# Optimization experiments

Measured on AMD Instinct MI355X. Metric: run time of the kernel, lower is better.

The kernel has to match this reference:

```python
import jax, jax.numpy as jnp
import numpy as np
import math

B, S, H, NH, HD, RD, INNER, MAXPOS, EPS = 2, 2048, 4096, 16, 256, 64, 16384, 2048, 1e-5


def setup_inputs() -> dict:
    key = jax.random.key(0)
    ks = jax.random.split(key, 8)
    sd = 0.02
    return {
        "hidden_states": jax.random.normal(ks[0], (B, S, H), jnp.float32),
        "attention_mask": jnp.ones((B, S), jnp.int32),
        "position_ids": jnp.broadcast_to(jnp.arange(S, dtype=jnp.int32), (B, S)),
        "ln_scale": jnp.ones((H,), jnp.float32),
        "ln_bias": jnp.zeros((H,), jnp.float32),
        "wq": jax.random.normal(ks[1], (H, H), jnp.float32) * sd,
        "wk": jax.random.normal(ks[2], (H, H), jnp.float32) * sd,
        "wv": jax.random.normal(ks[3], (H, H), jnp.float32) * sd,
        "wo": jax.random.normal(ks[4], (H, H), jnp.float32) * sd,
        "w_in": jax.random.normal(ks[5], (H, INNER), jnp.float32) * sd,
        "b_in": jnp.zeros((INNER,), jnp.float32),
        "w_out": jax.random.normal(ks[6], (INNER, H), jnp.float32) * sd,
        "b_out": jnp.zeros((H,), jnp.float32),
    }


def _rotate_every_two(t):
    # interleave (-odd, even) pairs along last dim
    r = jnp.stack((-t[..., 1::2], t[..., ::2]), axis=-1)
    return r.reshape(t.shape)


def reference(hidden_states, attention_mask, position_ids, ln_scale, ln_bias,
              wq, wk, wv, wo, w_in, b_in, w_out, b_out):
    x = hidden_states
    # LayerNorm (single ln feeds both attn and mlp in GPT-J parallel block)
    mu = jnp.mean(x, axis=-1, keepdims=True)
    var = jnp.mean(jnp.square(x - mu), axis=-1, keepdims=True)
    h = (x - mu) * jax.lax.rsqrt(var + EPS) * ln_scale + ln_bias

    # QKV projections (no bias), split heads: [B,S,NH,HD]
    q = (h @ wq).reshape(B, S, NH, HD)
    k = (h @ wk).reshape(B, S, NH, HD)
    v = (h @ wv).reshape(B, S, NH, HD)

    # sinusoidal table over rotary_dim, gathered by position_ids
    pos = jnp.arange(MAXPOS, dtype=jnp.float32)
    inv_freq = 1.0 / (10000.0 ** (jnp.arange(0, RD, 2, dtype=jnp.float32) / RD))
    freqs = pos[:, None] * inv_freq[None, :]          # [MAXPOS, RD//2]
    table = jnp.concatenate([jnp.sin(freqs), jnp.cos(freqs)], axis=-1)  # [MAXPOS, RD]
    sincos = table[position_ids]                      # [B,S,RD]
    sin, cos = jnp.split(sincos, 2, axis=-1)          # each [B,S,RD//2]
    sinr = jnp.repeat(sin[:, :, None, :], 2, axis=3)  # [B,S,1,RD]
    cosr = jnp.repeat(cos[:, :, None, :], 2, axis=3)

    def rope(t):
        return t * cosr + _rotate_every_two(t) * sinr

    q = jnp.concatenate([rope(q[..., :RD]), q[..., RD:]], axis=-1)
    k = jnp.concatenate([rope(k[..., :RD]), k[..., RD:]], axis=-1)

    # combined causal + padding mask -> additive bias
    causal = jnp.tril(jnp.ones((S, S), dtype=bool))
    mask = (attention_mask[:, None, None, :] > 0) & causal[None, None, :, :]
    bias = jnp.where(mask, 0.0, jnp.finfo(jnp.float32).min)  # [B,1,S,S]

    scale = 1.0 / math.sqrt(HD)
    scores = jnp.einsum('bqhd,bkhd->bhqk', q, k) * scale + bias
    attn = jax.nn.softmax(scores, axis=-1)
    ctx = jnp.einsum('bhqk,bkhd->bqhd', attn, v).reshape(B, S, H)
    attn_out = ctx @ wo

    # MLP on the same LN output (parallel residual), gelu_new ~ tanh gelu
    mlp = jax.nn.gelu(h @ w_in + b_in, approximate=True) @ w_out + b_out

    return x + attn_out + mlp
```

## Files before the change

### kernel.cpp

```cpp
#include <hip/hip_runtime.h>
#include <hip/hip_bf16.h>
#include <math.h>

namespace {

constexpr int kB = 2;
constexpr int kS = 2048;
constexpr int kH = 4096;
constexpr int kNH = 16;
constexpr int kHD = 256;
constexpr int kLDQ = 12288;

typedef __attribute__((ext_vector_type(4))) float f32x4;
typedef __attribute__((ext_vector_type(8))) short bf16x8;

__device__ __forceinline__ unsigned short f2bf(float f) {
  unsigned int u = __float_as_uint(f);
  u += 0x7FFFu + ((u >> 16) & 1u);
  return (unsigned short)(u >> 16);
}
__device__ __forceinline__ float bf2f(unsigned short h) {
  return __uint_as_float(((unsigned int)h) << 16);
}
__device__ __forceinline__ void gl2lds16(const void* g, void* l) {
  __builtin_amdgcn_global_load_lds(
      (const __attribute__((address_space(1))) unsigned int*)g,
      (__attribute__((address_space(3))) unsigned int*)l, 16, 0, 0);
}

#define SBAR asm volatile("s_barrier" ::: "memory")
#define LGKM0 asm volatile("s_waitcnt lgkmcnt(0)" ::: "memory")

__global__ __launch_bounds__(256) void ln_fwd(
    const float* __restrict__ x, const float* __restrict__ gam,
    const float* __restrict__ bet, unsigned short* __restrict__ hout,
    float* __restrict__ outp) {
  int row = blockIdx.x;
  int t = threadIdx.x;
  const float4* xr = (const float4*)(x + (size_t)row * kH);
  float4 v[4];
  float sum = 0.f, sq = 0.f;
#pragma unroll
  for (int i = 0; i < 4; i++) {
    v[i] = xr[t + i * 256];
    sum += v[i].x + v[i].y + v[i].z + v[i].w;
    sq += v[i].x * v[i].x + v[i].y * v[i].y + v[i].z * v[i].z + v[i].w * v[i].w;
  }
#pragma unroll
  for (int o = 32; o > 0; o >>= 1) {
    sum += __shfl_xor(sum, o);
    sq += __shfl_xor(sq, o);
  }
  __shared__ float red[8];
  if ((t & 63) == 0) { red[t >> 6] = sum; red[4 + (t >> 6)] = sq; }
  __syncthreads();
  sum = red[0] + red[1] + red[2] + red[3];
  sq = red[4] + red[5] + red[6] + red[7];
  float mu = sum * (1.f / kH);
  float rstd = rsqrtf(sq * (1.f / kH) - mu * mu + 1e-5f);
  const float4* gp = (const float4*)gam;
  const float4* bp = (const float4*)bet;
  ushort4* hr = (ushort4*)(hout + (size_t)row * kH);
  float4* orow = (float4*)(outp + (size_t)row * kH);
#pragma unroll
  for (int i = 0; i < 4; i++) {
    float4 g = gp[t + i * 256];
    float4 bb = bp[t + i * 256];
    ushort4 hv;
    hv.x = f2bf((v[i].x - mu) * rstd * g.x + bb.x);
    hv.y = f2bf((v[i].y - mu) * rstd * g.y + bb.y);
    hv.z = f2bf((v[i].z - mu) * rstd * g.z + bb.z);
    hv.w = f2bf((v[i].w - mu) * rstd * g.w + bb.w);
    hr[t + i * 256] = hv;
    orow[t + i * 256] = v[i];
  }
}

__global__ __launch_bounds__(256) void cvt_t(
    const float* __restrict__ in, int ldin, unsigned short* __restrict__ outp,
    int ldout) {
  __shared__ float tile[32][33];
  int n0 = blockIdx.x * 32, k0 = blockIdx.y * 32;
  int tx = threadIdx.x, ty = threadIdx.y;
#pragma unroll
  for (int i = 0; i < 4; i++)
    tile[ty + i * 8][tx] = in[(size_t)(k0 + ty + i * 8) * ldin + n0 + tx];
  __syncthreads();
#pragma unroll
  for (int i = 0; i < 4; i++)
    outp[(size_t)(n0 + ty + i * 8) * ldout + k0 + tx] =
        f2bf(tile[tx][ty + i * 8]);
}

__global__ __launch_bounds__(256) void vtrans(
    const unsigned short* __restrict__ qkv, unsigned short* __restrict__ vt) {
  __shared__ unsigned short tile[32][33];
  int bh = blockIdx.z;
  int s0 = blockIdx.x * 32, d0 = blockIdx.y * 32;
  int tx = threadIdx.x, ty = threadIdx.y;
  int b = bh >> 4, h = bh & 15;
  const unsigned short* src =
      qkv + (size_t)(b * kS) * kLDQ + 8192 + h * kHD;
#pragma unroll
  for (int i = 0; i < 4; i++)
    tile[ty + i * 8][tx] = src[(size_t)(s0 + ty + i * 8) * kLDQ + d0 + tx];
  __syncthreads();
  unsigned short* dst = vt + (size_t)bh * kHD * kS;
#pragma unroll
  for (int i = 0; i < 4; i++)
    dst[(size_t)(d0 + ty + i * 8) * kS + s0 + tx] = tile[tx][ty + i * 8];
}

__global__ __launch_bounds__(256) void rope_scale(
    unsigned short* __restrict__ qkv, const int* __restrict__ pos) {
  int idx = blockIdx.x * 256 + threadIdx.x;
  int j = idx & 127;
  int rowh = idx >> 7;
  int h = rowh & 15;
  int s = (rowh >> 4) & 2047;
  int b = rowh >> 15;
  size_t off = ((size_t)(b * kS + s)) * kLDQ + h * kHD + 2 * j;
  const float SCALE = 0.0625f;
  if (j < 32) {
    int p = pos[b * kS + s];
    float inv = exp2f(-(float)j * (13.287712379549449f / 32.f));
    float fr = (float)p * inv;
    float sn, cs;
    sincosf(fr, &sn, &cs);
    float e = bf2f(qkv[off]), o = bf2f(qkv[off + 1]);
    qkv[off] = f2bf((e * cs - o * sn) * SCALE);
    qkv[off + 1] = f2bf((o * cs + e * sn) * SCALE);
    e = bf2f(qkv[off + 4096]); o = bf2f(qkv[off + 4097]);
    qkv[off + 4096] = f2bf(e * cs - o * sn);
    qkv[off + 4097] = f2bf(o * cs + e * sn);
  } else {
    qkv[off] = f2bf(bf2f(qkv[off]) * SCALE);
    qkv[off + 1] = f2bf(bf2f(qkv[off + 1]) * SCALE);
  }
}

#define AF_MMA(P)                                                           \
  {                                                                         \
    bf16x8 af_[2][2];                                                       \
    _Pragma("unroll") for (int fm = 0; fm < 2; fm++)                        \
        _Pragma("unroll") for (int kk = 0; kk < 2; kk++) {                  \
      int q_ = (2 * (P) + fm) * 16 + l15;                                   \
      af_[fm][kk] = *(const bf16x8*)(cur + ((q_ & 64) << 8) + wm * 8192 +   \
                                     ((q_ & 63) << 7) +                     \
                                     ((((kk << 2) | l4) ^ key) << 4));      \
    }                                                                       \
    __builtin_amdgcn_s_setprio(1);                                          \
    _Pragma("unroll") for (int fm = 0; fm < 2; fm++)                        \
        _Pragma("unroll") for (int fn = 0; fn < 4; fn++)                    \
            _Pragma("unroll") for (int kk = 0; kk < 2; kk++)                \
      acc[2 * (P) + fm][fn] = __builtin_amdgcn_mfma_f32_16x16x32_bf16(      \
          af_[fm][kk], bfr[fn][kk], acc[2 * (P) + fm][fn], 0, 0, 0);        \
    __builtin_amdgcn_s_setprio(0);                                          \
  }

template <int EPI>
__global__ __launch_bounds__(512, 2) void gemm256(
    const unsigned short* __restrict__ A, int lda,
    const unsigned short* __restrict__ Bt, int ldb, void* __restrict__ Cp,
    int ldc, const float* __restrict__ bias, int K, int gx) {
  __shared__ __align__(16) char lds[131072];
  const int t = threadIdx.x;
  const int lane = t & 63, w = t >> 6;
  const int wm = w >> 2, wn = w & 3;
  const int l15 = lane & 15, l4 = lane >> 4;
  const int key = l15 & 7;

  const int nwg = gridDim.x;
  const int orig = blockIdx.x;
  const int wg = (orig & 7) * (nwg >> 3) + (orig >> 3);
  const int bx = wg % gx, by = wg / gx;
  const int m0 = by * 256, n0 = bx * 256;

  const int lr = t >> 3, ch = t & 7;
  const int swk = (ch ^ (lr & 7)) * 8;
  const unsigned short* aE0 = A + (size_t)(m0 + lr) * lda + swk;
  const unsigned short* aE1 = A + (size_t)(m0 + 128 + lr) * lda + swk;
  const unsigned short* aL0 = A + (size_t)(m0 + 64 + lr) * lda + swk;
  const unsigned short* aL1 = A + (size_t)(m0 + 192 + lr) * lda + swk;
  const unsigned short* b00 = Bt + (size_t)(n0 + lr) * ldb + swk;
  const unsigned short* b01 = Bt + (size_t)(n0 + 64 + lr) * ldb + swk;
  const unsigned short* b10 = Bt + (size_t)(n0 + 128 + lr) * ldb + swk;
  const unsigned short* b11 = Bt + (size_t)(n0 + 192 + lr) * ldb + swk;
  const int t16 = t * 16;

  f32x4 acc[8][4];
#pragma unroll
  for (int m = 0; m < 8; m++)
#pragma unroll
    for (int n = 0; n < 4; n++) acc[m][n] = (f32x4)(0.f);

  {
    char* b = lds;
    gl2lds16(b00, b + 32768 + t16); b00 += 64;
    gl2lds16(b01, b + 40960 + t16); b01 += 64;
    gl2lds16(b10, b + 49152 + t16); b10 += 64;
    gl2lds16(b11, b + 57344 + t16); b11 += 64;
    gl2lds16(aE0, b + t16);         aE0 += 64;
    gl2lds16(aE1, b + 8192 + t16);  aE1 += 64;
    gl2lds16(aL0, b + 16384 + t16); aL0 += 64;
    gl2lds16(aL1, b + 24576 + t16); aL1 += 64;
  }
  asm volatile("s_waitcnt vmcnt(2)" ::: "memory");
  SBAR;

  const int nt = K >> 6;
  for (int kt = 0; kt < nt; ++kt) {
    const char* cur = lds + (kt & 1) * 65536;
    char* nxt = lds + (((kt & 1) ^ 1)) * 65536;
    const bool pre = (kt + 1 < nt);
    bf16x8 bfr[4][2];
    if (pre) {
      gl2lds16(b00, nxt + 32768 + t16); b00 += 64;
      gl2lds16(b01, nxt + 40960 + t16); b01 += 64;
      gl2lds16(b10, nxt + 49152 + t16); b10 += 64;
      gl2lds16(b11, nxt + 57344 + t16); b11 += 64;
    }
#pragma unroll
    for (int fn = 0; fn < 4; fn++)
#pragma unroll
      for (int kk = 0; kk < 2; kk++) {
        int n = wn * 64 + fn * 16 + l15;
        bfr[fn][kk] = *(const bf16x8*)(cur + 32768 + (n << 7) +
                                       ((((kk << 2) | l4) ^ key) << 4));
      }
    AF_MMA(0)
    if (pre) {
      gl2lds16(aE0, nxt + t16);         aE0 += 64;
      gl2lds16(aE1, nxt + 8192 + t16);  aE1 += 64;
      gl2lds16(aL0, nxt + 16384 + t16); aL0 += 64;
      gl2lds16(aL1, nxt + 24576 + t16); aL1 += 64;
    }
    AF_MMA(1)
    if (pre) asm volatile("s_waitcnt vmcnt(8)" ::: "memory");
    else     asm volatile("s_waitcnt vmcnt(0)" ::: "memory");
    SBAR;
    AF_MMA(2)
    AF_MMA(3)
    LGKM0;
    if (pre) asm volatile("s_waitcnt vmcnt(2)" ::: "memory");
    SBAR;
  }

  const int crow = m0 + wm * 128 + l4 * 4;
  const int ccol = n0 + wn * 64 + l15;
#pragma unroll
  for (int m = 0; m < 8; m++) {
#pragma unroll
    for (int n = 0; n < 4; n++) {
      int col = ccol + n * 16;
#pragma unroll
      for (int r = 0; r < 4; r++) {
        int row = crow + m * 16 + r;
        float v = acc[m][n][r];
        size_t idx = (size_t)row * ldc + col;
        if constexpr (EPI == 0) {
          ((unsigned short*)Cp)[idx] = f2bf(v);
        } else if constexpr (EPI == 1) {
          float u = v + bias[col];
          float c = 0.7978845608028654f * (u + 0.044715f * u * u * u);
          float g = u / (1.0f + __expf(-2.0f * c));
          ((unsigned short*)Cp)[idx] = f2bf(g);
        } else if constexpr (EPI == 2) {
          ((float*)Cp)[idx] += v;
        } else {
          ((float*)Cp)[idx] += v + bias[col];
        }
      }
    }
  }
}

__global__ __launch_bounds__(512) void attn_fwd(
    const unsigned short* __restrict__ qkv, const unsigned short* __restrict__ vt,
    const int* __restrict__ amask, unsigned short* __restrict__ ctx) {
  __shared__ __align__(16) char alds[147456];
  const int t = threadIdx.x, lane = t & 63, w = t >> 6;
  const int bid = blockIdx.x;
  const int qb = 15 - (bid >> 5);
  const int bh = bid & 31;
  const int b = bh >> 4, h = bh & 15;
  const int l15 = lane & 15, l4 = lane >> 4;
  const int qbase = qb * 128;

  bf16x8 qf[8];
  {
    int qrow = qbase + w * 16 + l15;
    const unsigned short* qp =
        qkv + (size_t)(b * kS + qrow) * kLDQ + h * kHD + l4 * 8;
#pragma unroll
    for (int ks = 0; ks < 8; ks++) qf[ks] = *(const bf16x8*)(qp + ks * 32);
  }
  f32x4 o[16];
#pragma unroll
  for (int nf = 0; nf < 16; nf++) o[nf] = (f32x4)(0.f);
  float mr[4] = {-INFINITY, -INFINITY, -INFINITY, -INFINITY};
  float lr[4] = {0.f, 0.f, 0.f, 0.f};

  const unsigned short* kbase =
      qkv + (size_t)(b * kS) * kLDQ + 4096 + h * kHD;
  const unsigned short* vbase = vt + (size_t)bh * kHD * kS;
  unsigned short* sPw = (unsigned short*)(alds + 131072 + w * 2048);
  const int nt = 2 * qb + 2;

  const int krow = t >> 5, kch = t & 31;
  const int kcs = (kch ^ (krow & 7)) * 8;
  const int vrow = t >> 3, vch = t & 7;
  const int vcs = (vch ^ (vrow & 7)) * 8;
  const int t16b = t * 16;

#define ATTN_STAGE(KV0, BUF)                                                 \
  {                                                                          \
    char* kd = alds + (BUF) * 32768;                                         \
    char* vd = alds + 65536 + (BUF) * 32768;                                 \
    _Pragma("unroll") for (int i = 0; i < 4; i++) {                          \
      gl2lds16(kbase + (size_t)((KV0) + krow + i * 16) * kLDQ + kcs,         \
               kd + i * 8192 + t16b);                                        \
      gl2lds16(vbase + (size_t)(vrow + i * 64) * kS + (KV0) + vcs,           \
               vd + i * 8192 + t16b);                                        \
    }                                                                        \
  }

  ATTN_STAGE(0, 0)

  for (int kvt = 0; kvt < nt; kvt++) {
    const int kv0 = kvt * 64;
    const int cb = kvt & 1;
    if (kvt + 1 < nt) {
      ATTN_STAGE(kv0 + 64, cb ^ 1)
      asm volatile("s_waitcnt vmcnt(8)" ::: "memory");
    } else {
      asm volatile("s_waitcnt vmcnt(0)" ::: "memory");
    }
    asm volatile("s_barrier" ::: "memory");

    const unsigned short* sK = (const unsigned short*)(alds + cb * 32768);
    const unsigned short* sV =
        (const unsigned short*)(alds + 65536 + cb * 32768);

    f32x4 sc[4];
#pragma unroll
    for (int g = 0; g < 4; g++) sc[g] = (f32x4)(0.f);
    __builtin_amdgcn_s_setprio(1);
#pragma unroll
    for (int g = 0; g < 4; g++) {
      int row = g * 16 + l15;
#pragma unroll
      for (int ks = 0; ks < 8; ks++) {
        bf16x8 kf =
            *(const bf16x8*)&sK[row * 256 + (((ks * 4 + l4) ^ (row & 7)) * 8)];
        sc[g] = __builtin_amdgcn_mfma_f32_16x16x32_bf16(qf[ks], kf, sc[g], 0, 0, 0);
      }
    }
    __builtin_amdgcn_s_setprio(0);

    int am[4];
#pragma unroll
    for (int g = 0; g < 4; g++) am[g] = amask[b * kS + kv0 + g * 16 + l15];
    float mx[4];
#pragma unroll
    for (int r = 0; r < 4; r++) {
      int qi = qbase + w * 16 + l4 * 4 + r;
      float a = -INFINITY;
#pragma unroll
      for (int g = 0; g < 4; g++) {
        bool ok = (kv0 + g * 16 + l15 <= qi) && (am[g] != 0);
        float s = ok ? sc[g][r] : -INFINITY;
        sc[g][r] = s;
        a = fmaxf(a, s);
      }
#pragma unroll
      for (int d = 1; d < 16; d <<= 1) a = fmaxf(a, __shfl_xor(a, d));
      mx[r] = a;
    }
    bool nd = false;
#pragma unroll
    for (int r = 0; r < 4; r++) nd |= (mx[r] > mr[r] + 8.f);
    if (__any(nd)) {
#pragma unroll
      for (int r = 0; r < 4; r++) {
        float nm = fmaxf(mr[r], mx[r]);
        float c = __expf(mr[r] - nm);
        lr[r] *= c;
        mr[r] = nm;
#pragma unroll
        for (int nf = 0; nf < 16; nf++) o[nf][r] *= c;
      }
    }
#pragma unroll
    for (int r = 0; r < 4; r++) {
      int prow = l4 * 4 + r;
      int pkey = (prow ^ (prow >> 2)) & 7;
      float rs = 0.f;
#pragma unroll
      for (int g = 0; g < 4; g++) {
        float p = __expf(sc[g][r] - mr[r]);
        rs += p;
        int kvl = g * 16 + l15;
        sPw[prow * 64 + (((kvl >> 3) ^ pkey) << 3) + (kvl & 7)] = f2bf(p);
      }
#pragma unroll
      for (int d = 1; d < 16; d <<= 1) rs += __shfl_xor(rs, d);
      lr[r] += rs;
    }
    asm volatile("s_waitcnt lgkmcnt(0)" ::: "memory");

    int rkey = (l15 ^ (l15 >> 2)) & 7;
    bf16x8 pa[2];
#pragma unroll
    for (int ks2 = 0; ks2 < 2; ks2++)
      pa[ks2] = *(const bf16x8*)&sPw[l15 * 64 + (((ks2 * 4 + l4) ^ rkey) << 3)];
    __builtin_amdgcn_s_setprio(1);
#pragma unroll
    for (int nf = 0; nf < 16; nf++) {
      int vr = nf * 16 + l15;
#pragma unroll
      for (int ks2 = 0; ks2 < 2; ks2++) {
        bf16x8 vf =
            *(const bf16x8*)&sV[vr * 64 + (((ks2 * 4 + l4) ^ (vr & 7)) * 8)];
        o[nf] = __builtin_amdgcn_mfma_f32_16x16x32_bf16(pa[ks2], vf, o[nf], 0, 0, 0);
      }
    }
    __builtin_amdgcn_s_setprio(0);
    asm volatile("s_barrier" ::: "memory");
  }

  float invl[4];
#pragma unroll
  for (int r = 0; r < 4; r++) invl[r] = 1.0f / lr[r];
#pragma unroll
  for (int nf = 0; nf < 16; nf++) {
    int d = nf * 16 + l15;
#pragma unroll
    for (int r = 0; r < 4; r++) {
      int qi = qbase + w * 16 + l4 * 4 + r;
      ctx[(size_t)(b * kS + qi) * kH + h * kHD + d] = f2bf(o[nf][r] * invl[r]);
    }
  }
#undef ATTN_STAGE
}

}

extern "C" void kernel_launch(void* const* d_in, const int* in_sizes, int n_in,
                              void* d_out, int out_size, void* d_ws,
                              size_t ws_size, hipStream_t stream) {
  const float* x = (const float*)d_in[0];
  const int* amask = (const int*)d_in[1];
  const int* pos = (const int*)d_in[2];
  const float* lns = (const float*)d_in[3];
  const float* lnb = (const float*)d_in[4];
  const float* wq = (const float*)d_in[5];
  const float* wk = (const float*)d_in[6];
  const float* wv = (const float*)d_in[7];
  const float* wo = (const float*)d_in[8];
  const float* w_in = (const float*)d_in[9];
  const float* b_in = (const float*)d_in[10];
  const float* w_out = (const float*)d_in[11];
  const float* b_out = (const float*)d_in[12];
  float* out = (float*)d_out;

  if (ws_size < 268435456ull) return;
  unsigned short* ws = (unsigned short*)d_ws;
  unsigned short* h_bf = ws;
  unsigned short* wqkvT = ws + 16777216;
  unsigned short* qkv = ws + 67108864;
  unsigned short* vtb = ws + 117440512;
  unsigned short* ctxb = ws + 16777216;
  unsigned short* woT = ws + 33554432;
  unsigned short* w_inT = ws + 33554432;
  unsigned short* mid = ws + 67108864;
  unsigned short* w_outT = ws;

  dim3 t256(256);
  dim3 t512(512);
  dim3 t32x8(32, 8);

  ln_fwd<<<kB * kS, t256, 0, stream>>>(x, lns, lnb, h_bf, out);

  cvt_t<<<dim3(128, 128), t32x8, 0, stream>>>(wq, 4096, wqkvT, 4096);
  cvt_t<<<dim3(128, 128), t32x8, 0, stream>>>(wk, 4096, wqkvT + 16777216, 4096);
  cvt_t<<<dim3(128, 128), t32x8, 0, stream>>>(wv, 4096, wqkvT + 33554432, 4096);
  gemm256<0><<<dim3(768), t512, 0, stream>>>(h_bf, 4096, wqkvT, 4096,
                                             qkv, kLDQ, nullptr, 4096, 48);
  rope_scale<<<32768, t256, 0, stream>>>(qkv, pos);
  vtrans<<<dim3(64, 8, 32), t32x8, 0, stream>>>(qkv, vtb);
  attn_fwd<<<dim3(512), t512, 0, stream>>>(qkv, vtb, amask, ctxb);
  cvt_t<<<dim3(128, 128), t32x8, 0, stream>>>(wo, 4096, woT, 4096);
  gemm256<2><<<dim3(256), t512, 0, stream>>>(ctxb, 4096, woT, 4096, out,
                                             4096, nullptr, 4096, 16);
  for (int c = 0; c < 2; c++) {
    cvt_t<<<dim3(256, 128), t32x8, 0, stream>>>(w_in + c * 8192, 16384, w_inT,
                                                4096);
    gemm256<1><<<dim3(512), t512, 0, stream>>>(
        h_bf, 4096, w_inT, 4096, mid + c * 8192, 16384, b_in + c * 8192, 4096,
        32);
  }
  cvt_t<<<dim3(128, 512), t32x8, 0, stream>>>(w_out, 4096, w_outT, 16384);
  gemm256<3><<<dim3(256), t512, 0, stream>>>(mid, 16384, w_outT, 16384, out,
                                             4096, b_out, 16384, 16);
}
```

Before: 1.945 ms.

## Add 128x256-tile GEMM kernel for QKV and MLP-in projections

Introduces a new gemm128 kernel with 256 threads, a 128x256 output tile, K-step 32 and double-buffered LDS loads with swizzled layout. It replaces gemm256 for the QKV projection and the two MLP-in chunks, doubling the number of workgroups. The aim is better occupancy and wave scheduling on the many CUs. The cost is lower per-block data reuse and more global traffic per FLOP. The simple per-iteration full vmcnt wait also limits how much load latency is hidden.

```diff
diff --git a/kernel.cpp b/kernel.cpp
--- a/kernel.cpp
+++ b/kernel.cpp
@@ -139,6 +139,113 @@
   }
 }
 
+template <int EPI>
+__global__ __launch_bounds__(256) void gemm128(
+    const unsigned short* __restrict__ A, int lda,
+    const unsigned short* __restrict__ Bt, int ldb, void* __restrict__ Cp,
+    int ldc, const float* __restrict__ bias, int K, int gx) {
+  __shared__ __align__(16) char lds[49152];
+  const int t = threadIdx.x;
+  const int lane = t & 63, w = t >> 6;
+  const int l15 = lane & 15, l4 = lane >> 4;
+
+  const int nwg = gridDim.x;
+  const int orig = blockIdx.x;
+  const int wg = (orig & 7) * (nwg >> 3) + (orig >> 3);
+  const int bx = wg % gx, by = wg / gx;
+  const int m0 = by * 128, n0 = bx * 256;
+
+  const unsigned short* sp[6];
+#pragma unroll
+  for (int i = 0; i < 6; i++) {
+    int g = i * 256 + t;
+    int q = (g < 512) ? g : (g - 512);
+    int p = q >> 3, s = (q & 7) ^ (p & 7);
+    int row = 2 * p + (s >> 2), chunk = s & 3;
+    sp[i] = ((g < 512) ? (A + (size_t)(m0 + row) * lda)
+                       : (Bt + (size_t)(n0 + row) * ldb)) +
+            chunk * 8;
+  }
+  const int t16 = t * 16;
+
+  const int swz = ((((l15 & 1) << 2) | l4) ^ ((l15 >> 1) & 7)) << 4;
+  const int abase = ((l15 >> 1) << 7) + swz;
+  const int bbase = 8192 + w * 4096 + ((l15 >> 1) << 7) + swz;
+
+  f32x4 acc[8][4];
+#pragma unroll
+  for (int m = 0; m < 8; m++)
+#pragma unroll
+    for (int n = 0; n < 4; n++) acc[m][n] = (f32x4)(0.f);
+
+#pragma unroll
+  for (int i = 0; i < 6; i++) {
+    gl2lds16(sp[i], lds + i * 4096 + t16);
+    sp[i] += 32;
+  }
+  asm volatile("s_waitcnt vmcnt(0)" ::: "memory");
+  SBAR;
+
+  const int nt = K >> 5;
+  for (int kt = 0; kt < nt; ++kt) {
+    if (kt + 1 < nt) {
+      char* dst = lds + ((kt + 1) & 1) * 24576;
+#pragma unroll
+      for (int i = 0; i < 6; i++) {
+        gl2lds16(sp[i], dst + i * 4096 + t16);
+        sp[i] += 32;
+      }
+    }
+    const char* cur = lds + (kt & 1) * 24576;
+    bf16x8 af[8], bv[4];
+#pragma unroll
+    for (int m = 0; m < 8; m++)
+      af[m] = *(const bf16x8*)(cur + abase + m * 1024);
+#pragma unroll
+    for (int n = 0; n < 4; n++)
+      bv[n] = *(const bf16x8*)(cur + bbase + n * 1024);
+    __builtin_amdgcn_s_setprio(1);
+#pragma unroll
+    for (int m = 0; m < 8; m++)
+#pragma unroll
+      for (int n = 0; n < 4; n++)
+        acc[m][n] = __builtin_amdgcn_mfma_f32_16x16x32_bf16(af[m], bv[n],
+                                                            acc[m][n], 0, 0, 0);
+    __builtin_amdgcn_s_setprio(0);
+    LGKM0;
+    asm volatile("s_waitcnt vmcnt(0)" ::: "memory");
+    SBAR;
+  }
+
+  const int crow = m0 + l4 * 4;
+  const int ccol = n0 + w * 64 + l15;
+#pragma unroll
+  for (int m = 0; m < 8; m++) {
+#pragma unroll
+    for (int n = 0; n < 4; n++) {
+      int col = ccol + n * 16;
+#pragma unroll
+      for (int r = 0; r < 4; r++) {
+        int row = crow + m * 16 + r;
+        float v = acc[m][n][r];
+        size_t idx = (size_t)row * ldc + col;
+        if constexpr (EPI == 0) {
+          ((unsigned short*)Cp)[idx] = f2bf(v);
+        } else if constexpr (EPI == 1) {
+          float u = v + bias[col];
+          float c = 0.7978845608028654f * (u + 0.044715f * u * u * u);
+          float g = u / (1.0f + __expf(-2.0f * c));
+          ((unsigned short*)Cp)[idx] = f2bf(g);
+        } else if constexpr (EPI == 2) {
+          ((float*)Cp)[idx] += v;
+        } else {
+          ((float*)Cp)[idx] += v + bias[col];
+        }
+      }
+    }
+  }
+}
+
 #define AF_MMA(P)                                                           \
   {                                                                         \
     bf16x8 af_[2][2];                                                       \
@@ -485,8 +592,8 @@
   cvt_t<<<dim3(128, 128), t32x8, 0, stream>>>(wq, 4096, wqkvT, 4096);
   cvt_t<<<dim3(128, 128), t32x8, 0, stream>>>(wk, 4096, wqkvT + 16777216, 4096);
   cvt_t<<<dim3(128, 128), t32x8, 0, stream>>>(wv, 4096, wqkvT + 33554432, 4096);
-  gemm256<0><<<dim3(768), t512, 0, stream>>>(h_bf, 4096, wqkvT, 4096,
-                                             qkv, kLDQ, nullptr, 4096, 48);
+  gemm128<0><<<dim3(1536), t256, 0, stream>>>(h_bf, 4096, wqkvT, 4096,
+                                              qkv, kLDQ, nullptr, 4096, 48);
   rope_scale<<<32768, t256, 0, stream>>>(qkv, pos);
   vtrans<<<dim3(64, 8, 32), t32x8, 0, stream>>>(qkv, vtb);
   attn_fwd<<<dim3(512), t512, 0, stream>>>(qkv, vtb, amask, ctxb);
@@ -496,7 +603,7 @@
   for (int c = 0; c < 2; c++) {
     cvt_t<<<dim3(256, 128), t32x8, 0, stream>>>(w_in + c * 8192, 16384, w_inT,
                                                 4096);
-    gemm256<1><<<dim3(512), t512, 0, stream>>>(
+    gemm128<1><<<dim3(1024), t256, 0, stream>>>(
         h_bf, 4096, w_inT, 4096, mid + c * 8192, 16384, b_in + c * 8192, 4096,
         32);
   }
```

Measured after the change: 2.846 ms. +46.3%, slower.
